# Kernel optimization log

Measured on AMD Instinct MI355X. Metric: run time of the kernel, lower is better.

## Reference

```python
import jax, jax.numpy as jnp
import numpy as np

B, N_NODES, E = 2, 4096, 16384
H, DQK, DV = 8, 16, 128
DV_HEAD = DV // H  # dim_v_head = dim_v // n_heads


def setup_inputs() -> dict:
    key = jax.random.key(0)
    k1, k2, k3, k4, k5 = jax.random.split(key, 5)
    return {
        "query_values": jax.random.normal(k1, (B, E, H * DQK), jnp.float32),
        "key_values": jax.random.normal(k2, (B, N_NODES, H * DQK), jnp.float32),
        "value_values": jax.random.normal(k3, (B, E, DV), jnp.float32),
        "query_indices": jax.random.randint(k4, (B, E, 2), 0, N_NODES, jnp.int32),
        "value_indices": jax.random.randint(k5, (B, E, 2), 0, N_NODES, jnp.int32),
    }


def _heads(x, d):
    # torch: stack(x.split(d, -1), 0)  => [N, H*d] -> [H, N, d], head-major chunks
    n = x.shape[0]
    return jnp.transpose(x.reshape(n, -1, d), (1, 0, 2))


def reference(query_values, key_values, value_values, query_indices, value_indices):
    b, eq, _ = query_values.shape
    n_nodes = key_values.shape[1]
    n = b * n_nodes                       # total nodes across batch
    nv = b * eq                           # total value/query edges (full mask)
    node_ofs = (jnp.arange(b, dtype=query_indices.dtype) * n_nodes)[:, None, None]

    # _concat_batch: masked flatten (mask all True) + per-head split
    q = _heads(query_values.reshape(nv, -1), DQK)       # [H, Nq, d]
    k = _heads(key_values.reshape(n, -1), DQK)          # [H, n,  d]
    v = _heads(value_values.reshape(nv, -1), DV_HEAD)   # [H, Nv, dv_head]

    # _partial_key_value_sum: gather keys at edge row index, outer product, scatter-add by col
    v_idx = (value_indices + node_ofs).reshape(nv, 2)
    row, col = v_idx[:, 0], v_idx[:, 1]
    k_g = k[:, row, :]                                  # [H, Nv, d]
    # cat(unbind(h),-1).flatten(1,2): layout (n, i*DV + h*DV_HEAD + j)
    kv = jnp.einsum('hni,hnj->nihj', k_g, v).reshape(nv, DQK * DV)
    kg_flat = jnp.transpose(k_g, (1, 0, 2)).reshape(nv, H * DQK)
    kv_k = jnp.concatenate([kv, kg_flat], axis=-1)      # [Nv, DQK*DV + H*DQK]
    kv_k = jax.ops.segment_sum(kv_k, col, num_segments=n)  # coo(...).coalesce().to_dense()

    # _partial_apply_graph_query with dim1=2: gather by query col index
    q_idx = (query_indices + node_ofs).reshape(nv, 2)[:, 1]
    g = kv_k[q_idx]                                     # [Nq, DQK*DV + H*DQK]
    kv_q = jnp.transpose(g[:, :DQK * DV].reshape(nv, DQK, H, DV_HEAD), (2, 0, 1, 3))  # [H,Nq,d,dvh]
    k_sum = jnp.transpose(g[:, DQK * DV:].reshape(nv, H, DQK), (1, 0, 2))             # [H,Nq,d]

    att = jnp.einsum('hni,hnij->hnj', q, kv_q)          # [H, Nq, dv_head]
    qk = jnp.einsum('hni,hni->hn', q, k_sum)[..., None]
    qk = jnp.where(qk == 0, jnp.asarray(1e-5, qk.dtype), qk)
    att = att / qk
    att = jnp.transpose(att, (1, 0, 2)).reshape(b, eq, DV)

    # zero self-loop query edges (ord_q == 2 path)
    loop_mask = (query_indices[..., 0] != query_indices[..., 1])[..., None]
    return jnp.where(loop_mask, att, jnp.zeros((), att.dtype))
```

## Files before the change

kernel.cpp:

```cpp
#include <hip/hip_runtime.h>

#define B_SZ     2
#define E_EDGES  16384
#define N_NODES  4096
#define NTOT     (B_SZ * N_NODES)
#define NV       (B_SZ * E_EDGES)
#define DVTOT    128
#define LOG2_E   14
#define CAP      32

#define ZERO_INT4 200704

__device__ __forceinline__ int padidx(int f) { return f + ((f >> 4) << 2); }

__global__ __launch_bounds__(256) void zero_ws(int4* __restrict__ p) {
    int i = blockIdx.x * blockDim.x + threadIdx.x;
    p[i] = make_int4(0, 0, 0, 0);
}

__global__ __launch_bounds__(256) void fill_split(
    const int* __restrict__ qidx,
    const int* __restrict__ vidx,
    int*  __restrict__ ecnt,
    int*  __restrict__ qcnt,
    int2* __restrict__ ebuf,
    int*  __restrict__ qbuf)
{
    int t = blockIdx.x * blockDim.x + threadIdx.x;
    if (t < NV) {
        int e = t;
        int ofs = (e >> LOG2_E) * N_NODES;
        int2 vi = ((const int2*)vidx)[e];
        int col = vi.y + ofs;
        int p = atomicAdd(&ecnt[col], 1);
        if (p < CAP) ebuf[col * CAP + p] = make_int2(e + 1, vi.x + ofs);
    } else {
        int e = t - NV;
        int ofs = (e >> LOG2_E) * N_NODES;
        int2 qi = ((const int2*)qidx)[e];
        int g  = qi.y + ofs;
        int pq = atomicAdd(&qcnt[g], 1);
        if (pq < CAP) qbuf[g * CAP + pq] = (e + 1) | ((qi.x == qi.y) ? 0x80000000 : 0);
    }
}

#define KACC(C, V)                                                       \
    {                                                                    \
        const float4* kp = (const float4*)&sk[wid][C][h20];              \
        float4 k0 = kp[0], k1 = kp[1], k2 = kp[2], k3 = kp[3];           \
        float kk[16] = {k0.x,k0.y,k0.z,k0.w, k1.x,k1.y,k1.z,k1.w,        \
                        k2.x,k2.y,k2.z,k2.w, k3.x,k3.y,k3.z,k3.w};       \
        _Pragma("unroll")                                                \
        for (int i = 0; i < 16; ++i) {                                   \
            ks[i]  += kk[i];                                             \
            kva[i] += kk[i] * (V).x;                                     \
            kvb[i] += kk[i] * (V).y;                                     \
        }                                                                \
    }

#define QOUT(C, TREG)                                                    \
    {                                                                    \
        const float4* qp = (const float4*)&sq[wid][C][h20];              \
        float4 q0 = qp[0], q1 = qp[1], q2 = qp[2], q3 = qp[3];           \
        float qq[16] = {q0.x,q0.y,q0.z,q0.w, q1.x,q1.y,q1.z,q1.w,        \
                        q2.x,q2.y,q2.z,q2.w, q3.x,q3.y,q3.z,q3.w};       \
        float sa = 0.0f, sb = 0.0f, w = 0.0f;                            \
        _Pragma("unroll")                                                \
        for (int i = 0; i < 16; ++i) {                                   \
            sa += qq[i] * kva[i];                                        \
            sb += qq[i] * kvb[i];                                        \
            w  += qq[i] * ks[i];                                         \
        }                                                                \
        float den = (w == 0.0f) ? 1e-5f : w;                             \
        float inv = 1.0f / den;                                          \
        float2 o;                                                        \
        o.x = ((TREG) < 0) ? 0.0f : sa * inv;                            \
        o.y = ((TREG) < 0) ? 0.0f : sb * inv;                            \
        *(float2*)(out + (size_t)(((TREG) & 0x7FFFFFFF) - 1) * DVTOT + f2) = o; \
    }

__global__ __launch_bounds__(256) void attn_node(
    const float* __restrict__ qv,
    const float* __restrict__ keys,
    const float* __restrict__ vals,
    const int2*  __restrict__ ebuf,
    const int*   __restrict__ qbuf,
    float*       __restrict__ out)
{
    __shared__ float sk[4][4][160];
    __shared__ float sq[4][4][160];

    int wid  = threadIdx.x >> 6;
    int lane = threadIdx.x & 63;
    int g    = __builtin_amdgcn_readfirstlane(blockIdx.x * 4 + wid);

    int h20 = (lane >> 3) * 20;
    int f2  = 2 * lane;
    int pf2 = padidx(f2);

    const int2* eb = ebuf + (size_t)g * CAP;
    const int*  qb = qbuf + (size_t)g * CAP;

    int qt[8]; int2 er[8];
#pragma unroll
    for (int c = 0; c < 8; ++c) { qt[c] = qb[c]; er[c] = eb[c]; }

    int nq0 = qt[0] ? (qt[1] ? (qt[2] ? (qt[3] ? 4 : 3) : 2) : 1) : 0;
    if (nq0 == 0) return;
    int dg0 = er[0].x ? (er[1].x ? (er[2].x ? (er[3].x ? 4 : 3) : 2) : 1) : 0;

    float2 vvv[4];
    if (dg0) {
#pragma unroll
        for (int c = 0; c < 4; ++c) {
            int2 rc = (c < dg0) ? er[c] : er[0];
            *(float2*)&sk[wid][c][pf2] =
                *(const float2*)(keys + (size_t)rc.y * DVTOT + f2);
            vvv[c] = *(const float2*)(vals + (size_t)(rc.x - 1) * DVTOT + f2);
        }
    }
#pragma unroll
    for (int c = 0; c < 4; ++c) {
        int tc = (c < nq0) ? qt[c] : qt[0];
        *(float2*)&sq[wid][c][pf2] =
            *(const float2*)(qv + (size_t)((tc & 0x7FFFFFFF) - 1) * DVTOT + f2);
    }
    __builtin_amdgcn_wave_barrier();

    float kva[16], kvb[16], ks[16];
#pragma unroll
    for (int i = 0; i < 16; ++i) { kva[i] = 0.0f; kvb[i] = 0.0f; ks[i] = 0.0f; }

#pragma unroll
    for (int c = 0; c < 4; ++c)
        if (c < dg0) KACC(c, vvv[c]);

    if (dg0 == 4) {
        int n1 = er[4].x ? (er[5].x ? (er[6].x ? (er[7].x ? 4 : 3) : 2) : 1) : 0;
        if (n1) {
            float2 vv[4];
#pragma unroll
            for (int c = 0; c < 4; ++c) {
                int2 rc = (c < n1) ? er[4 + c] : er[4];
                vv[c] = *(const float2*)(vals + (size_t)(rc.x - 1) * DVTOT + f2);
            }
            __builtin_amdgcn_wave_barrier();
#pragma unroll
            for (int c = 0; c < 4; ++c) {
                int2 rc = (c < n1) ? er[4 + c] : er[4];
                *(float2*)&sk[wid][c][pf2] =
                    *(const float2*)(keys + (size_t)rc.y * DVTOT + f2);
            }
            __builtin_amdgcn_wave_barrier();
#pragma unroll
            for (int c = 0; c < 4; ++c)
                if (c < n1) KACC(c, vv[c]);
            if (n1 == 4) {
                for (int base = 8; base < CAP; base += 4) {
                    int2 r[4];
#pragma unroll
                    for (int c = 0; c < 4; ++c) r[c] = eb[base + c];
                    int n = r[0].x ? (r[1].x ? (r[2].x ? (r[3].x ? 4 : 3) : 2) : 1) : 0;
                    if (n == 0) break;
                    float2 vr[4];
#pragma unroll
                    for (int c = 0; c < 4; ++c) {
                        int2 rc = (c < n) ? r[c] : r[0];
                        vr[c] = *(const float2*)(vals + (size_t)(rc.x - 1) * DVTOT + f2);
                    }
                    __builtin_amdgcn_wave_barrier();
#pragma unroll
                    for (int c = 0; c < 4; ++c) {
                        int2 rc = (c < n) ? r[c] : r[0];
                        *(float2*)&sk[wid][c][pf2] =
                            *(const float2*)(keys + (size_t)rc.y * DVTOT + f2);
                    }
                    __builtin_amdgcn_wave_barrier();
#pragma unroll
                    for (int c = 0; c < 4; ++c)
                        if (c < n) KACC(c, vr[c]);
                    if (n < 4) break;
                }
            }
        }
    }

#pragma unroll
    for (int c = 0; c < 4; ++c)
        if (c < nq0) QOUT(c, qt[c]);

    if (nq0 == 4) {
        int n1 = qt[4] ? (qt[5] ? (qt[6] ? (qt[7] ? 4 : 3) : 2) : 1) : 0;
        if (n1) {
            float2 q2[4];
#pragma unroll
            for (int c = 0; c < 4; ++c) {
                int tc = (c < n1) ? qt[4 + c] : qt[4];
                q2[c] = *(const float2*)(qv + (size_t)((tc & 0x7FFFFFFF) - 1) * DVTOT + f2);
            }
            __builtin_amdgcn_wave_barrier();
#pragma unroll
            for (int c = 0; c < 4; ++c)
                *(float2*)&sq[wid][c][pf2] = q2[c];
            __builtin_amdgcn_wave_barrier();
#pragma unroll
            for (int c = 0; c < 4; ++c)
                if (c < n1) QOUT(c, qt[4 + c]);
            if (n1 == 4) {
                for (int base = 8; base < CAP; base += 4) {
                    int t[4];
#pragma unroll
                    for (int c = 0; c < 4; ++c) t[c] = qb[base + c];
                    int n = t[0] ? (t[1] ? (t[2] ? (t[3] ? 4 : 3) : 2) : 1) : 0;
                    if (n == 0) break;
                    float2 qr[4];
#pragma unroll
                    for (int c = 0; c < 4; ++c) {
                        int tc = (c < n) ? t[c] : t[0];
                        qr[c] = *(const float2*)(qv + (size_t)((tc & 0x7FFFFFFF) - 1) * DVTOT + f2);
                    }
                    __builtin_amdgcn_wave_barrier();
#pragma unroll
                    for (int c = 0; c < 4; ++c)
                        *(float2*)&sq[wid][c][pf2] = qr[c];
                    __builtin_amdgcn_wave_barrier();
#pragma unroll
                    for (int c = 0; c < 4; ++c)
                        if (c < n) QOUT(c, t[c]);
                    if (n < 4) break;
                }
            }
        }
    }
}

extern "C" void kernel_launch(void* const* d_in, const int* in_sizes, int n_in,
                              void* d_out, int out_size, void* d_ws, size_t ws_size,
                              hipStream_t stream) {
    const float* qv   = (const float*)d_in[0];
    const float* keys = (const float*)d_in[1];
    const float* vals = (const float*)d_in[2];
    const int*   qidx = (const int*)d_in[3];
    const int*   vidx = (const int*)d_in[4];
    float* out = (float*)d_out;

    char* ws = (char*)d_ws;
    int*  ecnt = (int*)ws;
    int*  qcnt = ecnt + NTOT;
    int2* ebuf = (int2*)(qcnt + NTOT);
    int*  qbuf = (int*)(ebuf + (size_t)NTOT * CAP);

    zero_ws<<<ZERO_INT4 / 256, 256, 0, stream>>>((int4*)ws);
    fill_split<<<(2 * NV) / 256, 256, 0, stream>>>(qidx, vidx, ecnt, qcnt, ebuf, qbuf);
    attn_node<<<NTOT / 4, 256, 0, stream>>>(qv, keys, vals, ebuf, qbuf, out);
}
```

Measured before the change: 30.91 us.

## Zero only counters, use counts instead of sentinel-scanned buckets, widen gathers

The workspace zeroing now clears only the two count arrays instead of the whole bucket storage. Bucket entries no longer carry a +1 sentinel, and the attention kernel reads the per-node counts to decide how many edges and queries to process, so stale bucket contents are never read. Key and query row gathers into shared memory switch from float2 per lane to float4 per half-wave. This removes a large memset pass and the zero-scan logic, at the cost of two extra count loads per wave.

```diff
diff --git a/kernel.cpp b/kernel.cpp
--- a/kernel.cpp
+++ b/kernel.cpp
@@ -9,11 +9,9 @@
 #define LOG2_E   14
 #define CAP      32
 
-#define ZERO_INT4 200704
-
 __device__ __forceinline__ int padidx(int f) { return f + ((f >> 4) << 2); }
 
-__global__ __launch_bounds__(256) void zero_ws(int4* __restrict__ p) {
+__global__ __launch_bounds__(256) void zero_counts(int4* __restrict__ p) {
     int i = blockIdx.x * blockDim.x + threadIdx.x;
     p[i] = make_int4(0, 0, 0, 0);
 }
@@ -33,14 +31,14 @@
         int2 vi = ((const int2*)vidx)[e];
         int col = vi.y + ofs;
         int p = atomicAdd(&ecnt[col], 1);
-        if (p < CAP) ebuf[col * CAP + p] = make_int2(e + 1, vi.x + ofs);
+        if (p < CAP) ebuf[col * CAP + p] = make_int2(e, vi.x + ofs);
     } else {
         int e = t - NV;
         int ofs = (e >> LOG2_E) * N_NODES;
         int2 qi = ((const int2*)qidx)[e];
         int g  = qi.y + ofs;
         int pq = atomicAdd(&qcnt[g], 1);
-        if (pq < CAP) qbuf[g * CAP + pq] = (e + 1) | ((qi.x == qi.y) ? 0x80000000 : 0);
+        if (pq < CAP) qbuf[g * CAP + pq] = e | ((qi.x == qi.y) ? 0x80000000 : 0);
     }
 }
 
@@ -76,13 +74,15 @@
         float2 o;                                                        \
         o.x = ((TREG) < 0) ? 0.0f : sa * inv;                            \
         o.y = ((TREG) < 0) ? 0.0f : sb * inv;                            \
-        *(float2*)(out + (size_t)(((TREG) & 0x7FFFFFFF) - 1) * DVTOT + f2) = o; \
+        *(float2*)(out + (size_t)((TREG) & 0x7FFFFFFF) * DVTOT + f2) = o; \
     }
 
 __global__ __launch_bounds__(256) void attn_node(
     const float* __restrict__ qv,
     const float* __restrict__ keys,
     const float* __restrict__ vals,
+    const int*   __restrict__ ecnt,
+    const int*   __restrict__ qcnt,
     const int2*  __restrict__ ebuf,
     const int*   __restrict__ qbuf,
     float*       __restrict__ out)
@@ -96,34 +96,46 @@
 
     int h20 = (lane >> 3) * 20;
     int f2  = 2 * lane;
-    int pf2 = padidx(f2);
+    int rsel = lane >> 5;
+    int col4 = (lane & 31) * 4;
+    int pcol4 = padidx(col4);
 
     const int2* eb = ebuf + (size_t)g * CAP;
     const int*  qb = qbuf + (size_t)g * CAP;
 
+    int nq = qcnt[g];
+    int dg = ecnt[g];
     int qt[8]; int2 er[8];
 #pragma unroll
     for (int c = 0; c < 8; ++c) { qt[c] = qb[c]; er[c] = eb[c]; }
 
-    int nq0 = qt[0] ? (qt[1] ? (qt[2] ? (qt[3] ? 4 : 3) : 2) : 1) : 0;
-    if (nq0 == 0) return;
-    int dg0 = er[0].x ? (er[1].x ? (er[2].x ? (er[3].x ? 4 : 3) : 2) : 1) : 0;
+    if (nq > CAP) nq = CAP;
+    if (dg > CAP) dg = CAP;
+    if (nq == 0) return;
+    int nq0 = nq < 4 ? nq : 4;
+    int dg0 = dg < 4 ? dg : 4;
 
     float2 vvv[4];
     if (dg0) {
 #pragma unroll
+        for (int p = 0; p < 2; ++p) {
+            int c = 2 * p + rsel;
+            int2 rc = (c < dg0) ? er[c] : er[0];
+            *(float4*)&sk[wid][c][pcol4] =
+                *(const float4*)(keys + (size_t)rc.y * DVTOT + col4);
+        }
+#pragma unroll
         for (int c = 0; c < 4; ++c) {
             int2 rc = (c < dg0) ? er[c] : er[0];
-            *(float2*)&sk[wid][c][pf2] =
-                *(const float2*)(keys + (size_t)rc.y * DVTOT + f2);
-            vvv[c] = *(const float2*)(vals + (size_t)(rc.x - 1) * DVTOT + f2);
-        }
-    }
-#pragma unroll
-    for (int c = 0; c < 4; ++c) {
+            vvv[c] = *(const float2*)(vals + (size_t)rc.x * DVTOT + f2);
+        }
+    }
+#pragma unroll
+    for (int p = 0; p < 2; ++p) {
+        int c = 2 * p + rsel;
         int tc = (c < nq0) ? qt[c] : qt[0];
-        *(float2*)&sq[wid][c][pf2] =
-            *(const float2*)(qv + (size_t)((tc & 0x7FFFFFFF) - 1) * DVTOT + f2);
+        *(float4*)&sq[wid][c][pcol4] =
+            *(const float4*)(qv + (size_t)(tc & 0x7FFFFFFF) * DVTOT + col4);
     }
     __builtin_amdgcn_wave_barrier();
 
@@ -135,53 +147,50 @@
     for (int c = 0; c < 4; ++c)
         if (c < dg0) KACC(c, vvv[c]);
 
-    if (dg0 == 4) {
-        int n1 = er[4].x ? (er[5].x ? (er[6].x ? (er[7].x ? 4 : 3) : 2) : 1) : 0;
-        if (n1) {
-            float2 vv[4];
+    if (dg > 4) {
+        int n1 = dg - 4; if (n1 > 4) n1 = 4;
+        float2 vv[4];
+#pragma unroll
+        for (int c = 0; c < 4; ++c) {
+            int2 rc = (c < n1) ? er[4 + c] : er[4];
+            vv[c] = *(const float2*)(vals + (size_t)rc.x * DVTOT + f2);
+        }
+        __builtin_amdgcn_wave_barrier();
+#pragma unroll
+        for (int p = 0; p < 2; ++p) {
+            int c = 2 * p + rsel;
+            int2 rc = (c < n1) ? er[4 + c] : er[4];
+            *(float4*)&sk[wid][c][pcol4] =
+                *(const float4*)(keys + (size_t)rc.y * DVTOT + col4);
+        }
+        __builtin_amdgcn_wave_barrier();
+#pragma unroll
+        for (int c = 0; c < 4; ++c)
+            if (c < n1) KACC(c, vv[c]);
+
+        for (int base = 8; base < dg; base += 4) {
+            int n = dg - base; if (n > 4) n = 4;
+            int2 r[4];
+#pragma unroll
+            for (int c = 0; c < 4; ++c) if (c < n) r[c] = eb[base + c];
+            float2 vr[4];
 #pragma unroll
             for (int c = 0; c < 4; ++c) {
-                int2 rc = (c < n1) ? er[4 + c] : er[4];
-                vv[c] = *(const float2*)(vals + (size_t)(rc.x - 1) * DVTOT + f2);
-            }
-            __builtin_amdgcn_wave_barrier();
-#pragma unroll
-            for (int c = 0; c < 4; ++c) {
-                int2 rc = (c < n1) ? er[4 + c] : er[4];
-                *(float2*)&sk[wid][c][pf2] =
-                    *(const float2*)(keys + (size_t)rc.y * DVTOT + f2);
+                int2 rc = (c < n) ? r[c] : r[0];
+                vr[c] = *(const float2*)(vals + (size_t)rc.x * DVTOT + f2);
+            }
+            __builtin_amdgcn_wave_barrier();
+#pragma unroll
+            for (int p = 0; p < 2; ++p) {
+                int c = 2 * p + rsel;
+                int2 rc = (c < n) ? r[c] : r[0];
+                *(float4*)&sk[wid][c][pcol4] =
+                    *(const float4*)(keys + (size_t)rc.y * DVTOT + col4);
             }
             __builtin_amdgcn_wave_barrier();
 #pragma unroll
             for (int c = 0; c < 4; ++c)
-                if (c < n1) KACC(c, vv[c]);
-            if (n1 == 4) {
-                for (int base = 8; base < CAP; base += 4) {
-                    int2 r[4];
-#pragma unroll
-                    for (int c = 0; c < 4; ++c) r[c] = eb[base + c];
-                    int n = r[0].x ? (r[1].x ? (r[2].x ? (r[3].x ? 4 : 3) : 2) : 1) : 0;
-                    if (n == 0) break;
-                    float2 vr[4];
-#pragma unroll
-                    for (int c = 0; c < 4; ++c) {
-                        int2 rc = (c < n) ? r[c] : r[0];
-                        vr[c] = *(const float2*)(vals + (size_t)(rc.x - 1) * DVTOT + f2);
-                    }
-                    __builtin_amdgcn_wave_barrier();
-#pragma unroll
-                    for (int c = 0; c < 4; ++c) {
-                        int2 rc = (c < n) ? r[c] : r[0];
-                        *(float2*)&sk[wid][c][pf2] =
-                            *(const float2*)(keys + (size_t)rc.y * DVTOT + f2);
-                    }
-                    __builtin_amdgcn_wave_barrier();
-#pragma unroll
-                    for (int c = 0; c < 4; ++c)
-                        if (c < n) KACC(c, vr[c]);
-                    if (n < 4) break;
-                }
-            }
+                if (c < n) KACC(c, vr[c]);
         }
     }
 
@@ -189,47 +198,48 @@
     for (int c = 0; c < 4; ++c)
         if (c < nq0) QOUT(c, qt[c]);
 
-    if (nq0 == 4) {
-        int n1 = qt[4] ? (qt[5] ? (qt[6] ? (qt[7] ? 4 : 3) : 2) : 1) : 0;
-        if (n1) {
-            float2 q2[4];
-#pragma unroll
-            for (int c = 0; c < 4; ++c) {
-                int tc = (c < n1) ? qt[4 + c] : qt[4];
-                q2[c] = *(const float2*)(qv + (size_t)((tc & 0x7FFFFFFF) - 1) * DVTOT + f2);
+    if (nq > 4) {
+        int n1 = nq - 4; if (n1 > 4) n1 = 4;
+        float4 q2[2];
+#pragma unroll
+        for (int p = 0; p < 2; ++p) {
+            int c = 2 * p + rsel;
+            int tc = (c < n1) ? qt[4 + c] : qt[4];
+            q2[p] = *(const float4*)(qv + (size_t)(tc & 0x7FFFFFFF) * DVTOT + col4);
+        }
+        __builtin_amdgcn_wave_barrier();
+#pragma unroll
+        for (int p = 0; p < 2; ++p) {
+            int c = 2 * p + rsel;
+            *(float4*)&sq[wid][c][pcol4] = q2[p];
+        }
+        __builtin_amdgcn_wave_barrier();
+#pragma unroll
+        for (int c = 0; c < 4; ++c)
+            if (c < n1) QOUT(c, qt[4 + c]);
+
+        for (int base = 8; base < nq; base += 4) {
+            int n = nq - base; if (n > 4) n = 4;
+            int t[4];
+#pragma unroll
+            for (int c = 0; c < 4; ++c) if (c < n) t[c] = qb[base + c];
+            float4 qr[2];
+#pragma unroll
+            for (int p = 0; p < 2; ++p) {
+                int c = 2 * p + rsel;
+                int tc = (c < n) ? t[c] : t[0];
+                qr[p] = *(const float4*)(qv + (size_t)(tc & 0x7FFFFFFF) * DVTOT + col4);
+            }
+            __builtin_amdgcn_wave_barrier();
+#pragma unroll
+            for (int p = 0; p < 2; ++p) {
+                int c = 2 * p + rsel;
+                *(float4*)&sq[wid][c][pcol4] = qr[p];
             }
             __builtin_amdgcn_wave_barrier();
 #pragma unroll
             for (int c = 0; c < 4; ++c)
-                *(float2*)&sq[wid][c][pf2] = q2[c];
-            __builtin_amdgcn_wave_barrier();
-#pragma unroll
-            for (int c = 0; c < 4; ++c)
-                if (c < n1) QOUT(c, qt[4 + c]);
-            if (n1 == 4) {
-                for (int base = 8; base < CAP; base += 4) {
-                    int t[4];
-#pragma unroll
-                    for (int c = 0; c < 4; ++c) t[c] = qb[base + c];
-                    int n = t[0] ? (t[1] ? (t[2] ? (t[3] ? 4 : 3) : 2) : 1) : 0;
-                    if (n == 0) break;
-                    float2 qr[4];
-#pragma unroll
-                    for (int c = 0; c < 4; ++c) {
-                        int tc = (c < n) ? t[c] : t[0];
-                        qr[c] = *(const float2*)(qv + (size_t)((tc & 0x7FFFFFFF) - 1) * DVTOT + f2);
-                    }
-                    __builtin_amdgcn_wave_barrier();
-#pragma unroll
-                    for (int c = 0; c < 4; ++c)
-                        *(float2*)&sq[wid][c][pf2] = qr[c];
-                    __builtin_amdgcn_wave_barrier();
-#pragma unroll
-                    for (int c = 0; c < 4; ++c)
-                        if (c < n) QOUT(c, t[c]);
-                    if (n < 4) break;
-                }
-            }
+                if (c < n) QOUT(c, t[c]);
         }
     }
 }
@@ -250,7 +260,7 @@
     int2* ebuf = (int2*)(qcnt + NTOT);
     int*  qbuf = (int*)(ebuf + (size_t)NTOT * CAP);
 
-    zero_ws<<<ZERO_INT4 / 256, 256, 0, stream>>>((int4*)ws);
+    zero_counts<<<16, 256, 0, stream>>>((int4*)ws);
     fill_split<<<(2 * NV) / 256, 256, 0, stream>>>(qidx, vidx, ecnt, qcnt, ebuf, qbuf);
-    attn_node<<<NTOT / 4, 256, 0, stream>>>(qv, keys, vals, ebuf, qbuf, out);
-}
+    attn_node<<<NTOT / 4, 256, 0, stream>>>(qv, keys, vals, ecnt, qcnt, ebuf, qbuf, out);
+}
```

Result: slower. 36.22 us (+17.2%).
